# Kernel optimization log

Measured on AMD Instinct MI355X. Metric: run time of the kernel, lower is better.

## Reference

```python
import jax, jax.numpy as jnp
import numpy as np

K_MASK = -2.3819763e+38
NUM_KV_HEADS = 4
SOFT_CAP = 50.0
WINDOW = 1024
ROPE_BASE = 10000.0
ROPE_SCALE = 1.0


def rms_norm(x, scale=None, eps=1e-6):
    var = jnp.mean(jnp.square(x), axis=-1, keepdims=True)
    normed = x * jax.lax.rsqrt(var + eps)
    if scale is not None:
        normed = normed * (1.0 + scale)
    return normed


def apply_rope(x, positions):
    # x: [B, T, N, H], positions: [B, T]
    head_dim = x.shape[-1]
    fraction = 2.0 * jnp.arange(head_dim // 2, dtype=jnp.float32) / head_dim
    timescale = ROPE_BASE ** fraction  # [H/2]
    sinusoid = positions[..., None, None].astype(jnp.float32) / timescale / ROPE_SCALE  # [B,T,1,H/2]
    sin, cos = jnp.sin(sinusoid), jnp.cos(sinusoid)
    first, second = jnp.split(x, 2, axis=-1)
    return jnp.concatenate([first * cos - second * sin,
                            second * cos + first * sin], axis=-1).astype(x.dtype)


def setup_inputs() -> dict:
    key = jax.random.key(0)
    ks = jax.random.split(key, 8)
    B, T, D, N, K, H, F = 2, 2048, 2048, 8, NUM_KV_HEADS, 256, 8192
    CACHE = 4096
    x = jax.random.normal(ks[0], (B, T, D), dtype=jnp.float32)
    segment_pos = jnp.broadcast_to(jnp.arange(T, dtype=jnp.int32)[None, :], (B, T))
    # causal mask over cache slots: after scatter, slot s (< T) holds position s; slots >= T are empty
    s_idx = jnp.arange(CACHE)
    t_idx = jnp.arange(T)
    attn_mask = (s_idx[None, :] <= t_idx[:, None]) & (s_idx[None, :] < T)
    attn_mask = jnp.broadcast_to(attn_mask[None], (B, T, CACHE))
    cache_k = jnp.zeros((B, CACHE, K, H), dtype=jnp.float32)
    cache_v = jnp.zeros((B, CACHE, K, H), dtype=jnp.float32)
    cache_positions = jnp.zeros((B, CACHE), dtype=jnp.int32)
    end_index = jnp.zeros((B,), dtype=jnp.int32)
    w_q = jax.random.normal(ks[1], (N, D, H), dtype=jnp.float32) * 0.02
    w_kv = jax.random.normal(ks[2], (2, K, D, H), dtype=jnp.float32) * 0.02
    w_attn_vec = jax.random.normal(ks[3], (N, H, D), dtype=jnp.float32) * 0.02
    w_gating = jax.random.normal(ks[4], (2, F, D), dtype=jnp.float32) * 0.02
    w_linear = jax.random.normal(ks[5], (F, D), dtype=jnp.float32) * 0.02
    return {
        'x': x, 'segment_pos': segment_pos, 'attn_mask': attn_mask,
        'cache_k': cache_k, 'cache_v': cache_v,
        'cache_positions': cache_positions, 'end_index': end_index,
        'w_q': w_q, 'w_kv': w_kv, 'w_attn_vec': w_attn_vec,
        'q_norm_scale': jnp.zeros((H,), dtype=jnp.float32),
        'k_norm_scale': jnp.zeros((H,), dtype=jnp.float32),
        'pre_attn_scale': jnp.zeros((D,), dtype=jnp.float32),
        'post_attn_scale': jnp.zeros((D,), dtype=jnp.float32),
        'pre_ffw_scale': jnp.zeros((D,), dtype=jnp.float32),
        'post_ffw_scale': jnp.zeros((D,), dtype=jnp.float32),
        'w_gating': w_gating, 'w_linear': w_linear,
        'skip_scale': jnp.ones((1,), dtype=jnp.float32),
    }


def reference(x, segment_pos, attn_mask, cache_k, cache_v, cache_positions, end_index,
              w_q, w_kv, w_attn_vec, q_norm_scale, k_norm_scale,
              pre_attn_scale, post_attn_scale, pre_ffw_scale, post_ffw_scale,
              w_gating, w_linear, skip_scale):
    B, T, D = x.shape
    cache_size = cache_v.shape[1]

    h = rms_norm(x, pre_attn_scale)

    # --- attention ---
    q = jnp.einsum('BTD,NDH->BTNH', h, w_q)
    q = rms_norm(q, q_norm_scale)
    q = apply_rope(q, segment_pos)

    k, v = jnp.einsum('BSD,CKDH->CBSKH', h, w_kv)
    k = rms_norm(k, k_norm_scale)
    v = rms_norm(v, None)
    k = apply_rope(k, segment_pos)

    # KV-cache scatter (ring-buffer indexing)
    idx = (end_index[:, None] + jnp.arange(T)[None, :]) % cache_size  # [B,T]
    bidx = jnp.arange(B)[:, None]
    v = cache_v.at[bidx, idx].set(v)              # [B,S,K,H]
    k = cache_k.at[bidx, idx].set(k)
    cache_pos = cache_positions.at[bidx, idx].set(segment_pos)  # [B,S]

    # GQA logits
    N, H = q.shape[2], q.shape[3]
    G = N // NUM_KV_HEADS
    qg = q.reshape(B, T, NUM_KV_HEADS, G, H)
    logits = jnp.einsum('BTKGH,BSKH->BTKGS', qg, k).reshape(B, T, N, cache_size)

    # soft cap
    logits = jnp.tanh(logits / SOFT_CAP) * SOFT_CAP

    # sliding-window mask against cache positions
    sliding = (cache_pos[:, None, :] > segment_pos[:, :, None] - WINDOW) & \
              (cache_pos[:, None, :] < segment_pos[:, :, None] + WINDOW)  # [B,T,S]
    mask = attn_mask & sliding

    padded = jnp.where(mask[:, :, None, :], logits, K_MASK)
    probs = jax.nn.softmax(padded, axis=-1).astype(k.dtype)

    pg = probs.reshape(B, T, NUM_KV_HEADS, G, cache_size)
    encoded = jnp.einsum('BTKGS,BSKH->BTKGH', pg, v).reshape(B, T, N, H)
    attn_out = jnp.einsum('BTNH,NHD->BTD', encoded, w_attn_vec)

    # post-attn norm + residual (skip_scale on the skip connection)
    attn_out = rms_norm(attn_out, post_attn_scale)
    attn_out = x * skip_scale + attn_out

    # --- feed-forward ---
    ffw_in = rms_norm(attn_out, pre_ffw_scale)
    gate = jnp.einsum('BTF,CHF->BTCH', ffw_in, w_gating)  # C=2
    act = jax.nn.gelu(gate[..., 0, :]) * gate[..., 1, :]
    ffw_out = jnp.einsum('BTH,HF->BTF', act, w_linear)
    ffw_out = rms_norm(ffw_out, post_ffw_scale)

    return attn_out + ffw_out
```

## Files before the change

### kernel.cpp

```cpp
#include <hip/hip_runtime.h>


typedef _Float16 h8 __attribute__((ext_vector_type(8)));
typedef _Float16 h4 __attribute__((ext_vector_type(4)));
typedef float f4 __attribute__((ext_vector_type(4)));

#define BDIM 2
#define TDIM 2048
#define DDIM 2048
#define NQ 8
#define NKV 4
#define HDIM 256
#define FDIM 8192
#define MROWS (BDIM * TDIM)
#define WINDOW 1024
#define QS 4096

__device__ __forceinline__ float gelu_fast(float x) {
  float u = 1.5957691216057308f * (x + 0.044715f * x * x * x);
  float e = __expf(u);
  return x * e / (e + 1.f);
}

__device__ __forceinline__ void g2l16(const _Float16* g, _Float16* l) {
  __builtin_amdgcn_global_load_lds(
      (const __attribute__((address_space(1))) void*)g,
      (__attribute__((address_space(3))) void*)l, 16, 0, 0);
}

__device__ inline float block_sum(float v, float* sbuf) {
#pragma unroll
  for (int off = 32; off; off >>= 1) v += __shfl_xor(v, off, 64);
  __syncthreads();
  if ((threadIdx.x & 63) == 0) sbuf[threadIdx.x >> 6] = v;
  __syncthreads();
  return sbuf[0] + sbuf[1] + sbuf[2] + sbuf[3];
}

template <int EPI>
__global__ __launch_bounds__(256, 3) void gemm_bt(
    const _Float16* __restrict__ A, const _Float16* __restrict__ Bt,
    void* __restrict__ Cout, int M, int Nc, int K) {
  __shared__ _Float16 As[2 * 128 * 32];
  __shared__ _Float16 Bs[2 * 128 * 32];
  const int tid = threadIdx.x;
  const int m0 = blockIdx.y * 128, n0 = blockIdx.x * 128;
  const int w = tid >> 6, lane = tid & 63;
  const int l16 = lane & 15, quad = lane >> 4;
  const int wm = (w >> 1) * 64, wn = (w & 1) * 64;

  f4 acc[4][4];
#pragma unroll
  for (int i = 0; i < 4; i++)
#pragma unroll
    for (int j = 0; j < 4; j++) {
      acc[i][j][0] = 0.f; acc[i][j][1] = 0.f; acc[i][j][2] = 0.f; acc[i][j][3] = 0.f;
    }

  const int lrow = lane >> 2, lcol = (lane & 3) * 8;
  const _Float16* Ag = A + (size_t)(m0 + w * 32 + lrow) * K + lcol;
  const _Float16* Bg = Bt + (size_t)(n0 + w * 32 + lrow) * K + lcol;
  _Float16* AsW = &As[w * 32 * 32];
  _Float16* BsW = &Bs[w * 32 * 32];

  for (int k0 = 0; k0 < K; k0 += 64) {
    __syncthreads();
#pragma unroll
    for (int s = 0; s < 2; s++) {
      g2l16(Ag + k0 + s * 32,                  AsW + s * 4096);
      g2l16(Ag + (size_t)16 * K + k0 + s * 32, AsW + s * 4096 + 16 * 32);
      g2l16(Bg + k0 + s * 32,                  BsW + s * 4096);
      g2l16(Bg + (size_t)16 * K + k0 + s * 32, BsW + s * 4096 + 16 * 32);
    }
    __syncthreads();
#pragma unroll
    for (int s = 0; s < 2; s++) {
      h8 af[4], bf[4];
#pragma unroll
      for (int i = 0; i < 4; i++)
        af[i] = *(const h8*)&As[s * 4096 + (wm + i * 16 + l16) * 32 + quad * 8];
#pragma unroll
      for (int i = 0; i < 4; i++)
        bf[i] = *(const h8*)&Bs[s * 4096 + (wn + i * 16 + l16) * 32 + quad * 8];
#pragma unroll
      for (int mi = 0; mi < 4; mi++)
#pragma unroll
        for (int ni = 0; ni < 4; ni++)
          acc[mi][ni] = __builtin_amdgcn_mfma_f32_16x16x32_f16(af[mi], bf[ni], acc[mi][ni], 0, 0, 0);
    }
  }

#pragma unroll
  for (int mi = 0; mi < 4; mi++)
#pragma unroll
    for (int ni = 0; ni < 4; ni++)
#pragma unroll
      for (int r = 0; r < 4; r++) {
        const int rg = m0 + wm + mi * 16 + quad * 4 + r;
        const int cg = n0 + wn + ni * 16 + l16;
        const size_t idx = (size_t)rg * Nc + cg;
        if (EPI == 0) ((float*)Cout)[idx] = acc[mi][ni][r];
        else          ((_Float16*)Cout)[idx] = (_Float16)acc[mi][ni][r];
      }
}

__global__ __launch_bounds__(256, 2) void gemm_gate(
    const _Float16* __restrict__ A, const _Float16* __restrict__ B0,
    const _Float16* __restrict__ B1, _Float16* __restrict__ act,
    int M, int Nc, int K) {
  __shared__ _Float16 As[2 * 128 * 32];
  __shared__ _Float16 Bs0[2 * 128 * 32];
  __shared__ _Float16 Bs1[2 * 128 * 32];
  const int tid = threadIdx.x;
  const int m0 = blockIdx.y * 128, n0 = blockIdx.x * 128;
  const int w = tid >> 6, lane = tid & 63;
  const int l16 = lane & 15, quad = lane >> 4;
  const int wm = (w >> 1) * 64, wn = (w & 1) * 64;

  f4 acc0[4][4], acc1[4][4];
#pragma unroll
  for (int i = 0; i < 4; i++)
#pragma unroll
    for (int j = 0; j < 4; j++) {
      acc0[i][j][0] = 0.f; acc0[i][j][1] = 0.f; acc0[i][j][2] = 0.f; acc0[i][j][3] = 0.f;
      acc1[i][j][0] = 0.f; acc1[i][j][1] = 0.f; acc1[i][j][2] = 0.f; acc1[i][j][3] = 0.f;
    }

  const int lrow = lane >> 2, lcol = (lane & 3) * 8;
  const _Float16* Ag  = A  + (size_t)(m0 + w * 32 + lrow) * K + lcol;
  const _Float16* B0g = B0 + (size_t)(n0 + w * 32 + lrow) * K + lcol;
  const _Float16* B1g = B1 + (size_t)(n0 + w * 32 + lrow) * K + lcol;
  _Float16* AsW  = &As[w * 32 * 32];
  _Float16* Bs0W = &Bs0[w * 32 * 32];
  _Float16* Bs1W = &Bs1[w * 32 * 32];

  for (int k0 = 0; k0 < K; k0 += 64) {
    __syncthreads();
#pragma unroll
    for (int s = 0; s < 2; s++) {
      g2l16(Ag + k0 + s * 32,                   AsW + s * 4096);
      g2l16(Ag + (size_t)16 * K + k0 + s * 32,  AsW + s * 4096 + 16 * 32);
      g2l16(B0g + k0 + s * 32,                  Bs0W + s * 4096);
      g2l16(B0g + (size_t)16 * K + k0 + s * 32, Bs0W + s * 4096 + 16 * 32);
      g2l16(B1g + k0 + s * 32,                  Bs1W + s * 4096);
      g2l16(B1g + (size_t)16 * K + k0 + s * 32, Bs1W + s * 4096 + 16 * 32);
    }
    __syncthreads();
#pragma unroll
    for (int s = 0; s < 2; s++) {
      h8 af[4], b0f[4], b1f[4];
#pragma unroll
      for (int i = 0; i < 4; i++)
        af[i] = *(const h8*)&As[s * 4096 + (wm + i * 16 + l16) * 32 + quad * 8];
#pragma unroll
      for (int i = 0; i < 4; i++) {
        b0f[i] = *(const h8*)&Bs0[s * 4096 + (wn + i * 16 + l16) * 32 + quad * 8];
        b1f[i] = *(const h8*)&Bs1[s * 4096 + (wn + i * 16 + l16) * 32 + quad * 8];
      }
#pragma unroll
      for (int mi = 0; mi < 4; mi++)
#pragma unroll
        for (int ni = 0; ni < 4; ni++) {
          acc0[mi][ni] = __builtin_amdgcn_mfma_f32_16x16x32_f16(af[mi], b0f[ni], acc0[mi][ni], 0, 0, 0);
          acc1[mi][ni] = __builtin_amdgcn_mfma_f32_16x16x32_f16(af[mi], b1f[ni], acc1[mi][ni], 0, 0, 0);
        }
    }
  }

#pragma unroll
  for (int mi = 0; mi < 4; mi++)
#pragma unroll
    for (int ni = 0; ni < 4; ni++)
#pragma unroll
      for (int r = 0; r < 4; r++) {
        const int rg = m0 + wm + mi * 16 + quad * 4 + r;
        const int cg = n0 + wn + ni * 16 + l16;
        act[(size_t)rg * Nc + cg] =
            (_Float16)(gelu_fast(acc0[mi][ni][r]) * acc1[mi][ni][r]);
      }
}

__global__ __launch_bounds__(256) void transpose_cast_kernel(
    const float* __restrict__ in, _Float16* __restrict__ out,
    int R, int C, size_t in_zstride, size_t out_zstride) {
  __shared__ float tile[64][65];
  const float* ip = in + blockIdx.z * in_zstride;
  _Float16* op = out + blockIdx.z * out_zstride;
  const int cb = blockIdx.x * 64, rb = blockIdx.y * 64;
  const int tx = threadIdx.x & 15, ty = threadIdx.x >> 4;
#pragma unroll
  for (int i = 0; i < 4; i++) {
    f4 v = *(const f4*)&ip[(size_t)(rb + ty + 16 * i) * C + cb + tx * 4];
    tile[ty + 16 * i][tx * 4 + 0] = v[0];
    tile[ty + 16 * i][tx * 4 + 1] = v[1];
    tile[ty + 16 * i][tx * 4 + 2] = v[2];
    tile[ty + 16 * i][tx * 4 + 3] = v[3];
  }
  __syncthreads();
#pragma unroll
  for (int i = 0; i < 4; i++) {
    const int c = ty + 16 * i;
    h4 o;
#pragma unroll
    for (int j = 0; j < 4; j++) o[j] = (_Float16)tile[tx * 4 + j][c];
    *(h4*)&op[(size_t)(cb + c) * R + rb + tx * 4] = o;
  }
}

__global__ void cast_fp16_kernel(const float* __restrict__ in,
                                 _Float16* __restrict__ out, int n4) {
  int i = blockIdx.x * 256 + threadIdx.x;
  if (i < n4) {
    f4 v = ((const f4*)in)[i];
    h4 o;
    o[0] = (_Float16)v[0]; o[1] = (_Float16)v[1];
    o[2] = (_Float16)v[2]; o[3] = (_Float16)v[3];
    ((h4*)out)[i] = o;
  }
}

__global__ __launch_bounds__(256) void rmsnorm_fp16_kernel(
    const float* __restrict__ in, const float* __restrict__ scale,
    _Float16* __restrict__ out) {
  __shared__ float sbuf[4];
  const int row = blockIdx.x, tid = threadIdx.x;
  const float* r = in + (size_t)row * 2048;
  f4 a = ((const f4*)r)[tid];
  f4 b = ((const f4*)r)[tid + 256];
  float ss = a[0]*a[0] + a[1]*a[1] + a[2]*a[2] + a[3]*a[3] +
             b[0]*b[0] + b[1]*b[1] + b[2]*b[2] + b[3]*b[3];
  float tot = block_sum(ss, sbuf);
  float rs = rsqrtf(tot * (1.f / 2048.f) + 1e-6f);
  f4 s0 = ((const f4*)scale)[tid];
  f4 s1 = ((const f4*)scale)[tid + 256];
  h4 o0, o1;
#pragma unroll
  for (int j = 0; j < 4; j++) {
    o0[j] = (_Float16)(a[j] * rs * (1.f + s0[j]));
    o1[j] = (_Float16)(b[j] * rs * (1.f + s1[j]));
  }
  ((h4*)(out + (size_t)row * 2048))[tid] = o0;
  ((h4*)(out + (size_t)row * 2048))[tid + 256] = o1;
}

__global__ __launch_bounds__(256) void headnorm_qkv_kernel(
    const _Float16* __restrict__ qkv, _Float16* __restrict__ out,
    const float* __restrict__ qsc, const float* __restrict__ ksc,
    const int* __restrict__ pos_arr) {
  const int inst = blockIdx.x * 4 + (threadIdx.x >> 6);
  const int lane = threadIdx.x & 63;
  const int row = inst >> 4, slot = inst & 15;
  const _Float16* r = qkv + (size_t)row * QS + slot * 256;
  h4 vh = ((const h4*)r)[lane];
  f4 v;
#pragma unroll
  for (int j = 0; j < 4; j++) v[j] = (float)vh[j];
  float ss = v[0]*v[0] + v[1]*v[1] + v[2]*v[2] + v[3]*v[3];
#pragma unroll
  for (int off = 32; off; off >>= 1) ss += __shfl_xor(ss, off, 64);
  const float rs = rsqrtf(ss * (1.f / 256.f) + 1e-6f);
  const float* scale = (slot < 8) ? qsc : (slot < 12 ? ksc : nullptr);
  f4 nv;
  if (scale) {
    f4 sc = ((const f4*)scale)[lane];
#pragma unroll
    for (int j = 0; j < 4; j++) nv[j] = v[j] * rs * (1.f + sc[j]);
  } else {
#pragma unroll
    for (int j = 0; j < 4; j++) nv[j] = v[j] * rs;
  }
  h4 res;
  if (slot < 12) {
    const float pos = (float)pos_arr[row];
    const bool lo = lane < 32;
#pragma unroll
    for (int j = 0; j < 4; j++) {
      float partner = __shfl_xor(nv[j], 32, 64);
      const int ph = (lane * 4 + j) & 127;
      float it = exp2f((float)ph * -0.103810253f);
      float ang = pos * it;
      float sn, cs;
      sincosf(ang, &sn, &cs);
      res[j] = (_Float16)(lo ? (nv[j] * cs - partner * sn)
                             : (nv[j] * cs + partner * sn));
    }
  } else {
#pragma unroll
    for (int j = 0; j < 4; j++) res[j] = (_Float16)nv[j];
  }
  ((h4*)(out + (size_t)row * QS + slot * 256))[lane] = res;
}

__global__ __launch_bounds__(256) void transpose_v_kernel(
    const _Float16* __restrict__ qkvh, _Float16* __restrict__ vT) {
  __shared__ _Float16 tile[32][33];
  const int z = blockIdx.z;
  const int b = z >> 2, kvh = z & 3;
  const int tb = blockIdx.x * 32, hb = blockIdx.y * 32;
  const int x = threadIdx.x, y = threadIdx.y;
#pragma unroll
  for (int i = 0; i < 4; i++)
    tile[y + 8 * i][x] =
        qkvh[(size_t)(b * TDIM + tb + y + 8 * i) * QS + 3072 + kvh * 256 + hb + x];
  __syncthreads();
#pragma unroll
  for (int i = 0; i < 4; i++)
    vT[((size_t)z * HDIM + hb + y + 8 * i) * TDIM + tb + x] = tile[x][y + 8 * i];
}

__global__ __launch_bounds__(256) void attn_kernel(
    const _Float16* __restrict__ qkvh, const _Float16* __restrict__ vT,
    _Float16* __restrict__ enc) {
  __shared__ _Float16 Ks[32 * 256];
  __shared__ _Float16 Vs[256 * 32];
  __shared__ _Float16 Ps[4][16 * 32];
  const int t0 = blockIdx.x * 64;
  const int n = blockIdx.y;
  const int b = blockIdx.z;
  const int kvh = n >> 1;
  const int tid = threadIdx.x;
  const int w = tid >> 6, lane = tid & 63, l16 = lane & 15, quad = lane >> 4;

  h8 qfrag[8];
  {
    const int trow = t0 + w * 16 + l16;
    const _Float16* qp =
        qkvh + (size_t)(b * TDIM + trow) * QS + n * HDIM + quad * 8;
#pragma unroll
    for (int ks = 0; ks < 8; ks++) qfrag[ks] = *(const h8*)(qp + ks * 32);
  }

  f4 O[16];
#pragma unroll
  for (int i = 0; i < 16; i++) { O[i][0] = 0.f; O[i][1] = 0.f; O[i][2] = 0.f; O[i][3] = 0.f; }
  float m_i[4], l_i[4];
#pragma unroll
  for (int r = 0; r < 4; r++) { m_i[r] = -1e30f; l_i[r] = 0.f; }

  int s_begin = t0 - (WINDOW - 1);
  if (s_begin < 0) s_begin = 0;
  s_begin &= ~31;
  const int s_end = t0 + 64;
  const _Float16* kbase = qkvh + (size_t)b * TDIM * QS + 2048 + kvh * HDIM;
  const _Float16* vbase = vT + ((size_t)(b * NKV + kvh) * HDIM) * TDIM;

  for (int s0 = s_begin; s0 < s_end; s0 += 32) {
    __syncthreads();
#pragma unroll
    for (int p = 0; p < 4; p++) {
      int g = p * 256 + tid;
      {
        int si = g >> 5, hg = (g & 31) << 3;
        *(h8*)&Ks[si * 256 + hg] = *(const h8*)(kbase + (size_t)(s0 + si) * QS + hg);
      }
      {
        int h = g >> 2, sg = (g & 3) << 3;
        *(h8*)&Vs[h * 32 + sg] = *(const h8*)(vbase + (size_t)h * TDIM + s0 + sg);
      }
    }
    __syncthreads();

    float P[2][4], cmax[4];
#pragma unroll
    for (int r = 0; r < 4; r++) cmax[r] = -1e30f;
#pragma unroll
    for (int sc = 0; sc < 2; sc++) {
      f4 lg; lg[0] = 0.f; lg[1] = 0.f; lg[2] = 0.f; lg[3] = 0.f;
#pragma unroll
      for (int ks = 0; ks < 8; ks++) {
        h8 kb = *(const h8*)&Ks[(sc * 16 + l16) * 256 + ks * 32 + quad * 8];
        lg = __builtin_amdgcn_mfma_f32_16x16x32_f16(qfrag[ks], kb, lg, 0, 0, 0);
      }
      const int scol = s0 + sc * 16 + l16;
#pragma unroll
      for (int r = 0; r < 4; r++) {
        const int trow = t0 + w * 16 + quad * 4 + r;
        float t = __expf(lg[r] * 0.04f);
        float xv = 50.f - 100.f * __builtin_amdgcn_rcpf(t + 1.f);
        bool valid = (scol <= trow) && (scol > trow - WINDOW);
        P[sc][r] = valid ? xv : -1e30f;
        cmax[r] = fmaxf(cmax[r], P[sc][r]);
      }
    }
#pragma unroll
    for (int off = 1; off < 16; off <<= 1)
#pragma unroll
      for (int r = 0; r < 4; r++) cmax[r] = fmaxf(cmax[r], __shfl_xor(cmax[r], off, 16));
    float alpha[4], psum[4];
#pragma unroll
    for (int r = 0; r < 4; r++) {
      float mnew = fmaxf(m_i[r], cmax[r]);
      alpha[r] = __expf(m_i[r] - mnew);
      m_i[r] = mnew;
      psum[r] = 0.f;
    }
#pragma unroll
    for (int sc = 0; sc < 2; sc++)
#pragma unroll
      for (int r = 0; r < 4; r++) {
        float pv = __expf(P[sc][r] - m_i[r]);
        P[sc][r] = pv;
        psum[r] += pv;
      }
#pragma unroll
    for (int off = 1; off < 16; off <<= 1)
#pragma unroll
      for (int r = 0; r < 4; r++) psum[r] += __shfl_xor(psum[r], off, 16);
#pragma unroll
    for (int r = 0; r < 4; r++) l_i[r] = l_i[r] * alpha[r] + psum[r];
#pragma unroll
    for (int i = 0; i < 16; i++)
#pragma unroll
      for (int r = 0; r < 4; r++) O[i][r] *= alpha[r];
#pragma unroll
    for (int sc = 0; sc < 2; sc++)
#pragma unroll
      for (int r = 0; r < 4; r++)
        Ps[w][(quad * 4 + r) * 32 + sc * 16 + l16] = (_Float16)P[sc][r];
    h8 pa = *(const h8*)&Ps[w][l16 * 32 + quad * 8];
#pragma unroll
    for (int ht = 0; ht < 16; ht++) {
      h8 vb = *(const h8*)&Vs[(ht * 16 + l16) * 32 + quad * 8];
      O[ht] = __builtin_amdgcn_mfma_f32_16x16x32_f16(pa, vb, O[ht], 0, 0, 0);
    }
  }

  float invl[4];
#pragma unroll
  for (int r = 0; r < 4; r++) invl[r] = 1.f / l_i[r];
#pragma unroll
  for (int ht = 0; ht < 16; ht++)
#pragma unroll
    for (int r = 0; r < 4; r++) {
      const int trow = t0 + w * 16 + quad * 4 + r;
      enc[((size_t)(b * TDIM + trow)) * (NQ * HDIM) + n * HDIM + ht * 16 + l16] =
          (_Float16)(O[ht][r] * invl[r]);
    }
}

__global__ __launch_bounds__(256) void postattn_kernel(
    const float* __restrict__ attnraw, const float* __restrict__ x,
    const float* __restrict__ post_scale, const float* __restrict__ pre_ffw_scale,
    const float* __restrict__ skip, float* __restrict__ attn_out,
    _Float16* __restrict__ ffw_in) {
  __shared__ float sbuf[4];
  const int row = blockIdx.x, tid = threadIdx.x;
  const float* ar = attnraw + (size_t)row * 2048;
  const float* xr = x + (size_t)row * 2048;
  f4 a0 = ((const f4*)ar)[tid], a1 = ((const f4*)ar)[tid + 256];
  float ss = a0[0]*a0[0] + a0[1]*a0[1] + a0[2]*a0[2] + a0[3]*a0[3] +
             a1[0]*a1[0] + a1[1]*a1[1] + a1[2]*a1[2] + a1[3]*a1[3];
  float tot = block_sum(ss, sbuf);
  float rs = rsqrtf(tot * (1.f / 2048.f) + 1e-6f);
  const float sk = skip[0];
  f4 x0 = ((const f4*)xr)[tid], x1 = ((const f4*)xr)[tid + 256];
  f4 p0 = ((const f4*)post_scale)[tid], p1 = ((const f4*)post_scale)[tid + 256];
  f4 at0, at1;
#pragma unroll
  for (int j = 0; j < 4; j++) {
    at0[j] = x0[j] * sk + a0[j] * rs * (1.f + p0[j]);
    at1[j] = x1[j] * sk + a1[j] * rs * (1.f + p1[j]);
  }
  ((f4*)(attn_out + (size_t)row * 2048))[tid] = at0;
  ((f4*)(attn_out + (size_t)row * 2048))[tid + 256] = at1;
  float ss2 = at0[0]*at0[0] + at0[1]*at0[1] + at0[2]*at0[2] + at0[3]*at0[3] +
              at1[0]*at1[0] + at1[1]*at1[1] + at1[2]*at1[2] + at1[3]*at1[3];
  float tot2 = block_sum(ss2, sbuf);
  float rs2 = rsqrtf(tot2 * (1.f / 2048.f) + 1e-6f);
  f4 f0 = ((const f4*)pre_ffw_scale)[tid], f1 = ((const f4*)pre_ffw_scale)[tid + 256];
  h4 o0, o1;
#pragma unroll
  for (int j = 0; j < 4; j++) {
    o0[j] = (_Float16)(at0[j] * rs2 * (1.f + f0[j]));
    o1[j] = (_Float16)(at1[j] * rs2 * (1.f + f1[j]));
  }
  ((h4*)(ffw_in + (size_t)row * 2048))[tid] = o0;
  ((h4*)(ffw_in + (size_t)row * 2048))[tid + 256] = o1;
}

__global__ __launch_bounds__(256) void final_kernel(
    const _Float16* __restrict__ ffw, const float* __restrict__ attn_out,
    const float* __restrict__ post_ffw_scale, float* __restrict__ out) {
  __shared__ float sbuf[4];
  const int row = blockIdx.x, tid = threadIdx.x;
  const _Float16* fr = ffw + (size_t)row * 2048;
  const float* ar = attn_out + (size_t)row * 2048;
  h4 fh0 = ((const h4*)fr)[tid], fh1 = ((const h4*)fr)[tid + 256];
  f4 a0, a1;
#pragma unroll
  for (int j = 0; j < 4; j++) { a0[j] = (float)fh0[j]; a1[j] = (float)fh1[j]; }
  float ss = a0[0]*a0[0] + a0[1]*a0[1] + a0[2]*a0[2] + a0[3]*a0[3] +
             a1[0]*a1[0] + a1[1]*a1[1] + a1[2]*a1[2] + a1[3]*a1[3];
  float tot = block_sum(ss, sbuf);
  float rs = rsqrtf(tot * (1.f / 2048.f) + 1e-6f);
  f4 s0 = ((const f4*)post_ffw_scale)[tid], s1 = ((const f4*)post_ffw_scale)[tid + 256];
  f4 x0 = ((const f4*)ar)[tid], x1 = ((const f4*)ar)[tid + 256];
  f4 o0, o1;
#pragma unroll
  for (int j = 0; j < 4; j++) {
    o0[j] = x0[j] + a0[j] * rs * (1.f + s0[j]);
    o1[j] = x1[j] + a1[j] * rs * (1.f + s1[j]);
  }
  ((f4*)(out + (size_t)row * 2048))[tid] = o0;
  ((f4*)(out + (size_t)row * 2048))[tid + 256] = o1;
}

extern "C" void kernel_launch(void* const* d_in, const int* in_sizes, int n_in,
                              void* d_out, int out_size, void* d_ws, size_t ws_size,
                              hipStream_t stream) {
  (void)in_sizes; (void)n_in; (void)out_size; (void)ws_size;
  const float* x              = (const float*)d_in[0];
  const int*   segment_pos    = (const int*)d_in[1];
  const float* w_q            = (const float*)d_in[7];
  const float* w_kv           = (const float*)d_in[8];
  const float* w_attn_vec     = (const float*)d_in[9];
  const float* q_norm_scale   = (const float*)d_in[10];
  const float* k_norm_scale   = (const float*)d_in[11];
  const float* pre_attn_scale = (const float*)d_in[12];
  const float* post_attn_scale= (const float*)d_in[13];
  const float* pre_ffw_scale  = (const float*)d_in[14];
  const float* post_ffw_scale = (const float*)d_in[15];
  const float* w_gating       = (const float*)d_in[16];
  const float* w_linear       = (const float*)d_in[17];
  const float* skip_scale     = (const float*)d_in[18];

  char* ws = (char*)d_ws;
  const size_t MB = 1024 * 1024;
  _Float16* Wqkv  = (_Float16*)(ws + 0);
  _Float16* Wo    = (_Float16*)(ws + 0);
  _Float16* Wg    = (_Float16*)(ws + 0);
  _Float16* Wl    = (_Float16*)(ws + 0);
  _Float16* Hbf   = (_Float16*)(ws + 64 * MB);
  float* attnF    = (float*)(ws + 80 * MB);
  _Float16* qkvraw= (_Float16*)(ws + 112 * MB);
  _Float16* qkvh  = (_Float16*)(ws + 144 * MB);
  _Float16* enc   = (_Float16*)(ws + 176 * MB);
  float* attnraw  = (float*)(ws + 192 * MB);
  _Float16* vT    = (_Float16*)(ws + 224 * MB);
  _Float16* act   = (_Float16*)(ws + 112 * MB);
  _Float16* ffw   = (_Float16*)(ws + 192 * MB);
  float* outp     = (float*)d_out;

  transpose_cast_kernel<<<dim3(HDIM / 64, DDIM / 64, NQ), 256, 0, stream>>>(
      w_q, Wqkv, DDIM, HDIM, (size_t)DDIM * HDIM, (size_t)HDIM * DDIM);
  transpose_cast_kernel<<<dim3(HDIM / 64, DDIM / 64, NKV), 256, 0, stream>>>(
      w_kv, Wqkv + (size_t)2048 * DDIM, DDIM, HDIM,
      (size_t)DDIM * HDIM, (size_t)HDIM * DDIM);
  transpose_cast_kernel<<<dim3(HDIM / 64, DDIM / 64, NKV), 256, 0, stream>>>(
      w_kv + (size_t)NKV * DDIM * HDIM, Wqkv + (size_t)3072 * DDIM, DDIM, HDIM,
      (size_t)DDIM * HDIM, (size_t)HDIM * DDIM);
  rmsnorm_fp16_kernel<<<MROWS, 256, 0, stream>>>(x, pre_attn_scale, Hbf);
  gemm_bt<1><<<dim3(QS / 128, MROWS / 128), 256, 0, stream>>>(
      Hbf, Wqkv, qkvraw, MROWS, QS, DDIM);
  headnorm_qkv_kernel<<<(MROWS * 16) / 4, 256, 0, stream>>>(
      qkvraw, qkvh, q_norm_scale, k_norm_scale, segment_pos);
  transpose_v_kernel<<<dim3(TDIM / 32, HDIM / 32, BDIM * NKV), dim3(32, 8), 0, stream>>>(
      qkvh, vT);
  attn_kernel<<<dim3(TDIM / 64, NQ, BDIM), 256, 0, stream>>>(qkvh, vT, enc);
  transpose_cast_kernel<<<dim3(DDIM / 64, (NQ * HDIM) / 64, 1), 256, 0, stream>>>(
      w_attn_vec, Wo, NQ * HDIM, DDIM, 0, 0);
  gemm_bt<0><<<dim3(DDIM / 128, MROWS / 128), 256, 0, stream>>>(
      enc, Wo, attnraw, MROWS, DDIM, NQ * HDIM);
  postattn_kernel<<<MROWS, 256, 0, stream>>>(attnraw, x, post_attn_scale,
                                             pre_ffw_scale, skip_scale, attnF, Hbf);
  cast_fp16_kernel<<<(2 * FDIM * DDIM / 4 + 255) / 256, 256, 0, stream>>>(
      w_gating, Wg, 2 * FDIM * DDIM / 4);
  gemm_gate<<<dim3(FDIM / 128, MROWS / 128), 256, 0, stream>>>(
      Hbf, Wg, Wg + (size_t)FDIM * DDIM, act, MROWS, FDIM, DDIM);
  transpose_cast_kernel<<<dim3(DDIM / 64, FDIM / 64, 1), 256, 0, stream>>>(
      w_linear, Wl, FDIM, DDIM, 0, 0);
  gemm_bt<1><<<dim3(DDIM / 128, MROWS / 128), 256, 0, stream>>>(
      act, Wl, ffw, MROWS, DDIM, FDIM);
  final_kernel<<<MROWS, 256, 0, stream>>>(ffw, attnF, post_ffw_scale, outp);
}
```

Baseline: 1.143 ms.

## Rewrite GEMMs as 256x128 triple-buffered swizzled 8-wave kernels; swizzle attention LDS

Replaces the 128x128 double-sync GEMM kernels with 512-thread 256-row tiles that keep a three-stage LDS ring. Global-to-LDS prefetch runs two k-steps ahead, split into phases interleaved with MFMA blocks, and raw s_barrier, s_setprio and explicit vmcnt waits hide load latency. LDS layouts are XOR-swizzled to avoid bank conflicts, and block IDs are remapped to group neighbouring tiles for L2 reuse. The attention kernel's K and V shared-memory tiles get the same XOR swizzle. The hand-tuned waitcnt and barrier ordering adds correctness risk, and the larger LDS footprint may reduce occupancy.

```diff
diff --git a/kernel.cpp b/kernel.cpp
--- a/kernel.cpp
+++ b/kernel.cpp
@@ -16,6 +16,8 @@
 #define WINDOW 1024
 #define QS 4096
 
+#define BAR() asm volatile("s_barrier" ::: "memory")
+
 __device__ __forceinline__ float gelu_fast(float x) {
   float u = 1.5957691216057308f * (x + 0.044715f * x * x * x);
   float e = __expf(u);
@@ -38,16 +40,35 @@
 }
 
 template <int EPI>
-__global__ __launch_bounds__(256, 3) void gemm_bt(
+__global__ __launch_bounds__(512, 2) void gemm256(
     const _Float16* __restrict__ A, const _Float16* __restrict__ Bt,
     void* __restrict__ Cout, int M, int Nc, int K) {
-  __shared__ _Float16 As[2 * 128 * 32];
-  __shared__ _Float16 Bs[2 * 128 * 32];
+  __shared__ _Float16 As[3][256 * 64];
+  __shared__ _Float16 Bs[3][128 * 64];
+  (void)M;
   const int tid = threadIdx.x;
-  const int m0 = blockIdx.y * 128, n0 = blockIdx.x * 128;
-  const int w = tid >> 6, lane = tid & 63;
+  const int lane = tid & 63, w = tid >> 6;
+  const int nwg = gridDim.x;
+  const int bid2 = (blockIdx.x & 7) * (nwg >> 3) + (blockIdx.x >> 3);
+  const int nbx = Nc >> 7;
+  const int bx = bid2 % nbx, by = bid2 / nbx;
+  const int m0 = by * 256, n0 = bx * 128;
+  const int wm = (w >> 1) * 64, wn = (w & 1) * 64;
   const int l16 = lane & 15, quad = lane >> 4;
-  const int wm = (w >> 1) * 64, wn = (w & 1) * 64;
+
+  const int lr = lane >> 3;
+  const int swz8 = ((lane & 7) ^ lr) << 3;
+  const _Float16* Ag = A + (size_t)(m0 + w * 32 + lr) * K + swz8;
+  const _Float16* Bg = Bt + (size_t)(n0 + w * 16 + lr) * K + swz8;
+
+  const int qs8 = (quad ^ (l16 & 3)) << 3;
+  const int kxo = ((l16 >> 2) & 1) << 5;
+  int aoff[4], boff[4];
+#pragma unroll
+  for (int i = 0; i < 4; i++) {
+    aoff[i] = (wm + i * 16 + l16) * 64 + qs8;
+    boff[i] = (wn + i * 16 + l16) * 64 + qs8;
+  }
 
   f4 acc[4][4];
 #pragma unroll
@@ -57,38 +78,69 @@
       acc[i][j][0] = 0.f; acc[i][j][1] = 0.f; acc[i][j][2] = 0.f; acc[i][j][3] = 0.f;
     }
 
-  const int lrow = lane >> 2, lcol = (lane & 3) * 8;
-  const _Float16* Ag = A + (size_t)(m0 + w * 32 + lrow) * K + lcol;
-  const _Float16* Bg = Bt + (size_t)(n0 + w * 32 + lrow) * K + lcol;
-  _Float16* AsW = &As[w * 32 * 32];
-  _Float16* BsW = &Bs[w * 32 * 32];
-
-  for (int k0 = 0; k0 < K; k0 += 64) {
-    __syncthreads();
-#pragma unroll
-    for (int s = 0; s < 2; s++) {
-      g2l16(Ag + k0 + s * 32,                  AsW + s * 4096);
-      g2l16(Ag + (size_t)16 * K + k0 + s * 32, AsW + s * 4096 + 16 * 32);
-      g2l16(Bg + k0 + s * 32,                  BsW + s * 4096);
-      g2l16(Bg + (size_t)16 * K + k0 + s * 32, BsW + s * 4096 + 16 * 32);
-    }
-    __syncthreads();
-#pragma unroll
-    for (int s = 0; s < 2; s++) {
-      h8 af[4], bf[4];
-#pragma unroll
-      for (int i = 0; i < 4; i++)
-        af[i] = *(const h8*)&As[s * 4096 + (wm + i * 16 + l16) * 32 + quad * 8];
-#pragma unroll
-      for (int i = 0; i < 4; i++)
-        bf[i] = *(const h8*)&Bs[s * 4096 + (wn + i * 16 + l16) * 32 + quad * 8];
-#pragma unroll
-      for (int mi = 0; mi < 4; mi++)
-#pragma unroll
-        for (int ni = 0; ni < 4; ni++)
-          acc[mi][ni] = __builtin_amdgcn_mfma_f32_16x16x32_f16(af[mi], bf[ni], acc[mi][ni], 0, 0, 0);
-    }
-  }
+#define SA(b, kt, c) g2l16(Ag + (size_t)(c) * 8 * K + (size_t)(kt) * 64, \
+                           &As[b][(w * 32 + (c) * 8) * 64])
+#define SB(b, kt, c) g2l16(Bg + (size_t)(c) * 8 * K + (size_t)(kt) * 64, \
+                           &Bs[b][(w * 16 + (c) * 8) * 64])
+
+  SA(0, 0, 0); SA(0, 0, 1); SA(0, 0, 2); SA(0, 0, 3); SB(0, 0, 0); SB(0, 0, 1);
+  SA(1, 1, 0); SA(1, 1, 1); SA(1, 1, 2); SA(1, 1, 3); SB(1, 1, 0); SB(1, 1, 1);
+  asm volatile("s_waitcnt vmcnt(6)" ::: "memory");
+  BAR();
+
+  const int nt = K >> 6;
+  for (int kt = 0; kt < nt; ++kt) {
+    const int cur = kt % 3, nb = (kt + 2) % 3;
+    const bool pf = (kt + 2) < nt;
+    const _Float16* Ab = As[cur];
+    const _Float16* Bb = Bs[cur];
+    h8 af[4][2], bf[4][2];
+#pragma unroll
+    for (int i = 0; i < 4; i++) {
+      af[i][0] = *(const h8*)&Ab[aoff[i] + kxo];
+      af[i][1] = *(const h8*)&Ab[aoff[i] + (kxo ^ 32)];
+    }
+#pragma unroll
+    for (int i = 0; i < 2; i++) {
+      bf[i][0] = *(const h8*)&Bb[boff[i] + kxo];
+      bf[i][1] = *(const h8*)&Bb[boff[i] + (kxo ^ 32)];
+    }
+    if (pf) { SA(nb, kt + 2, 0); SA(nb, kt + 2, 1); SA(nb, kt + 2, 2); }
+    BAR();
+    __builtin_amdgcn_s_setprio(1);
+#pragma unroll
+    for (int mi = 0; mi < 4; mi++)
+#pragma unroll
+      for (int ni = 0; ni < 2; ni++)
+#pragma unroll
+        for (int ks = 0; ks < 2; ks++)
+          acc[mi][ni] = __builtin_amdgcn_mfma_f32_16x16x32_f16(
+              af[mi][ks], bf[ni][ks], acc[mi][ni], 0, 0, 0);
+    __builtin_amdgcn_s_setprio(0);
+    BAR();
+#pragma unroll
+    for (int i = 2; i < 4; i++) {
+      bf[i][0] = *(const h8*)&Bb[boff[i] + kxo];
+      bf[i][1] = *(const h8*)&Bb[boff[i] + (kxo ^ 32)];
+    }
+    if (pf) { SA(nb, kt + 2, 3); SB(nb, kt + 2, 0); SB(nb, kt + 2, 1); }
+    BAR();
+    __builtin_amdgcn_s_setprio(1);
+#pragma unroll
+    for (int mi = 0; mi < 4; mi++)
+#pragma unroll
+      for (int ni = 2; ni < 4; ni++)
+#pragma unroll
+        for (int ks = 0; ks < 2; ks++)
+          acc[mi][ni] = __builtin_amdgcn_mfma_f32_16x16x32_f16(
+              af[mi][ks], bf[ni][ks], acc[mi][ni], 0, 0, 0);
+    __builtin_amdgcn_s_setprio(0);
+    if (pf)                 asm volatile("s_waitcnt vmcnt(6)" ::: "memory");
+    else if (kt + 2 == nt)  asm volatile("s_waitcnt vmcnt(0)" ::: "memory");
+    BAR();
+  }
+#undef SA
+#undef SB
 
 #pragma unroll
   for (int mi = 0; mi < 4; mi++)
@@ -104,73 +156,117 @@
       }
 }
 
-__global__ __launch_bounds__(256, 2) void gemm_gate(
+__global__ __launch_bounds__(512, 2) void gemm_gate256(
     const _Float16* __restrict__ A, const _Float16* __restrict__ B0,
     const _Float16* __restrict__ B1, _Float16* __restrict__ act,
     int M, int Nc, int K) {
-  __shared__ _Float16 As[2 * 128 * 32];
-  __shared__ _Float16 Bs0[2 * 128 * 32];
-  __shared__ _Float16 Bs1[2 * 128 * 32];
+  __shared__ _Float16 As[3][256 * 64];
+  __shared__ _Float16 B0s[3][64 * 64];
+  __shared__ _Float16 B1s[3][64 * 64];
+  (void)M;
   const int tid = threadIdx.x;
-  const int m0 = blockIdx.y * 128, n0 = blockIdx.x * 128;
-  const int w = tid >> 6, lane = tid & 63;
+  const int lane = tid & 63, w = tid >> 6;
+  const int nwg = gridDim.x;
+  const int bid2 = (blockIdx.x & 7) * (nwg >> 3) + (blockIdx.x >> 3);
+  const int nbx = Nc >> 6;
+  const int bx = bid2 % nbx, by = bid2 / nbx;
+  const int m0 = by * 256, n0 = bx * 64;
+  const int wm = (w >> 1) * 64, wn = (w & 1) * 32;
   const int l16 = lane & 15, quad = lane >> 4;
-  const int wm = (w >> 1) * 64, wn = (w & 1) * 64;
-
-  f4 acc0[4][4], acc1[4][4];
+
+  const int lr = lane >> 3;
+  const int swz8 = ((lane & 7) ^ lr) << 3;
+  const _Float16* Ag  = A  + (size_t)(m0 + w * 32 + lr) * K + swz8;
+  const _Float16* B0g = B0 + (size_t)(n0 + w * 8 + lr) * K + swz8;
+  const _Float16* B1g = B1 + (size_t)(n0 + w * 8 + lr) * K + swz8;
+
+  const int qs8 = (quad ^ (l16 & 3)) << 3;
+  const int kxo = ((l16 >> 2) & 1) << 5;
+  int aoff[4], boff[2];
+#pragma unroll
+  for (int i = 0; i < 4; i++) aoff[i] = (wm + i * 16 + l16) * 64 + qs8;
+#pragma unroll
+  for (int i = 0; i < 2; i++) boff[i] = (wn + i * 16 + l16) * 64 + qs8;
+
+  f4 acc0[4][2], acc1[4][2];
 #pragma unroll
   for (int i = 0; i < 4; i++)
 #pragma unroll
-    for (int j = 0; j < 4; j++) {
+    for (int j = 0; j < 2; j++) {
       acc0[i][j][0] = 0.f; acc0[i][j][1] = 0.f; acc0[i][j][2] = 0.f; acc0[i][j][3] = 0.f;
       acc1[i][j][0] = 0.f; acc1[i][j][1] = 0.f; acc1[i][j][2] = 0.f; acc1[i][j][3] = 0.f;
     }
 
-  const int lrow = lane >> 2, lcol = (lane & 3) * 8;
-  const _Float16* Ag  = A  + (size_t)(m0 + w * 32 + lrow) * K + lcol;
-  const _Float16* B0g = B0 + (size_t)(n0 + w * 32 + lrow) * K + lcol;
-  const _Float16* B1g = B1 + (size_t)(n0 + w * 32 + lrow) * K + lcol;
-  _Float16* AsW  = &As[w * 32 * 32];
-  _Float16* Bs0W = &Bs0[w * 32 * 32];
-  _Float16* Bs1W = &Bs1[w * 32 * 32];
-
-  for (int k0 = 0; k0 < K; k0 += 64) {
-    __syncthreads();
-#pragma unroll
-    for (int s = 0; s < 2; s++) {
-      g2l16(Ag + k0 + s * 32,                   AsW + s * 4096);
-      g2l16(Ag + (size_t)16 * K + k0 + s * 32,  AsW + s * 4096 + 16 * 32);
-      g2l16(B0g + k0 + s * 32,                  Bs0W + s * 4096);
-      g2l16(B0g + (size_t)16 * K + k0 + s * 32, Bs0W + s * 4096 + 16 * 32);
-      g2l16(B1g + k0 + s * 32,                  Bs1W + s * 4096);
-      g2l16(B1g + (size_t)16 * K + k0 + s * 32, Bs1W + s * 4096 + 16 * 32);
-    }
-    __syncthreads();
-#pragma unroll
-    for (int s = 0; s < 2; s++) {
-      h8 af[4], b0f[4], b1f[4];
-#pragma unroll
-      for (int i = 0; i < 4; i++)
-        af[i] = *(const h8*)&As[s * 4096 + (wm + i * 16 + l16) * 32 + quad * 8];
-#pragma unroll
-      for (int i = 0; i < 4; i++) {
-        b0f[i] = *(const h8*)&Bs0[s * 4096 + (wn + i * 16 + l16) * 32 + quad * 8];
-        b1f[i] = *(const h8*)&Bs1[s * 4096 + (wn + i * 16 + l16) * 32 + quad * 8];
-      }
-#pragma unroll
-      for (int mi = 0; mi < 4; mi++)
-#pragma unroll
-        for (int ni = 0; ni < 4; ni++) {
-          acc0[mi][ni] = __builtin_amdgcn_mfma_f32_16x16x32_f16(af[mi], b0f[ni], acc0[mi][ni], 0, 0, 0);
-          acc1[mi][ni] = __builtin_amdgcn_mfma_f32_16x16x32_f16(af[mi], b1f[ni], acc1[mi][ni], 0, 0, 0);
-        }
-    }
-  }
+#define SA(b, kt, c) g2l16(Ag + (size_t)(c) * 8 * K + (size_t)(kt) * 64, \
+                           &As[b][(w * 32 + (c) * 8) * 64])
+#define SB0(b, kt) g2l16(B0g + (size_t)(kt) * 64, &B0s[b][w * 8 * 64])
+#define SB1(b, kt) g2l16(B1g + (size_t)(kt) * 64, &B1s[b][w * 8 * 64])
+
+  SA(0, 0, 0); SA(0, 0, 1); SA(0, 0, 2); SA(0, 0, 3); SB0(0, 0); SB1(0, 0);
+  SA(1, 1, 0); SA(1, 1, 1); SA(1, 1, 2); SA(1, 1, 3); SB0(1, 1); SB1(1, 1);
+  asm volatile("s_waitcnt vmcnt(6)" ::: "memory");
+  BAR();
+
+  const int nt = K >> 6;
+  for (int kt = 0; kt < nt; ++kt) {
+    const int cur = kt % 3, nb = (kt + 2) % 3;
+    const bool pf = (kt + 2) < nt;
+    const _Float16* Ab = As[cur];
+    const _Float16* Bb0 = B0s[cur];
+    const _Float16* Bb1 = B1s[cur];
+    h8 af[4][2], b0f[2][2], b1f[2][2];
+#pragma unroll
+    for (int i = 0; i < 4; i++) {
+      af[i][0] = *(const h8*)&Ab[aoff[i] + kxo];
+      af[i][1] = *(const h8*)&Ab[aoff[i] + (kxo ^ 32)];
+    }
+#pragma unroll
+    for (int i = 0; i < 2; i++) {
+      b0f[i][0] = *(const h8*)&Bb0[boff[i] + kxo];
+      b0f[i][1] = *(const h8*)&Bb0[boff[i] + (kxo ^ 32)];
+    }
+    if (pf) { SA(nb, kt + 2, 0); SA(nb, kt + 2, 1); SA(nb, kt + 2, 2); }
+    BAR();
+    __builtin_amdgcn_s_setprio(1);
+#pragma unroll
+    for (int mi = 0; mi < 4; mi++)
+#pragma unroll
+      for (int ni = 0; ni < 2; ni++)
+#pragma unroll
+        for (int ks = 0; ks < 2; ks++)
+          acc0[mi][ni] = __builtin_amdgcn_mfma_f32_16x16x32_f16(
+              af[mi][ks], b0f[ni][ks], acc0[mi][ni], 0, 0, 0);
+    __builtin_amdgcn_s_setprio(0);
+    BAR();
+#pragma unroll
+    for (int i = 0; i < 2; i++) {
+      b1f[i][0] = *(const h8*)&Bb1[boff[i] + kxo];
+      b1f[i][1] = *(const h8*)&Bb1[boff[i] + (kxo ^ 32)];
+    }
+    if (pf) { SA(nb, kt + 2, 3); SB0(nb, kt + 2); SB1(nb, kt + 2); }
+    BAR();
+    __builtin_amdgcn_s_setprio(1);
+#pragma unroll
+    for (int mi = 0; mi < 4; mi++)
+#pragma unroll
+      for (int ni = 0; ni < 2; ni++)
+#pragma unroll
+        for (int ks = 0; ks < 2; ks++)
+          acc1[mi][ni] = __builtin_amdgcn_mfma_f32_16x16x32_f16(
+              af[mi][ks], b1f[ni][ks], acc1[mi][ni], 0, 0, 0);
+    __builtin_amdgcn_s_setprio(0);
+    if (pf)                 asm volatile("s_waitcnt vmcnt(6)" ::: "memory");
+    else if (kt + 2 == nt)  asm volatile("s_waitcnt vmcnt(0)" ::: "memory");
+    BAR();
+  }
+#undef SA
+#undef SB0
+#undef SB1
 
 #pragma unroll
   for (int mi = 0; mi < 4; mi++)
 #pragma unroll
-    for (int ni = 0; ni < 4; ni++)
+    for (int ni = 0; ni < 2; ni++)
 #pragma unroll
       for (int r = 0; r < 4; r++) {
         const int rg = m0 + wm + mi * 16 + quad * 4 + r;
@@ -320,6 +416,9 @@
   const int kvh = n >> 1;
   const int tid = threadIdx.x;
   const int w = tid >> 6, lane = tid & 63, l16 = lane & 15, quad = lane >> 4;
+  const int kxr = (l16 >> 2) & 1;
+  const int qsK8 = (quad ^ (l16 & 3)) << 3;
+  const int qsV8 = (quad ^ ((l16 >> 1) & 3)) << 3;
 
   h8 qfrag[8];
   {
@@ -350,12 +449,14 @@
     for (int p = 0; p < 4; p++) {
       int g = p * 256 + tid;
       {
-        int si = g >> 5, hg = (g & 31) << 3;
-        *(h8*)&Ks[si * 256 + hg] = *(const h8*)(kbase + (size_t)(s0 + si) * QS + hg);
+        int si = g >> 5, c = g & 31;
+        *(h8*)&Ks[si * 256 + ((c ^ (si & 7)) << 3)] =
+            *(const h8*)(kbase + (size_t)(s0 + si) * QS + (c << 3));
       }
       {
-        int h = g >> 2, sg = (g & 3) << 3;
-        *(h8*)&Vs[h * 32 + sg] = *(const h8*)(vbase + (size_t)h * TDIM + s0 + sg);
+        int h = g >> 2, c = g & 3;
+        *(h8*)&Vs[h * 32 + ((c ^ ((g >> 3) & 3)) << 3)] =
+            *(const h8*)(vbase + (size_t)h * TDIM + s0 + (c << 3));
       }
     }
     __syncthreads();
@@ -368,7 +469,7 @@
       f4 lg; lg[0] = 0.f; lg[1] = 0.f; lg[2] = 0.f; lg[3] = 0.f;
 #pragma unroll
       for (int ks = 0; ks < 8; ks++) {
-        h8 kb = *(const h8*)&Ks[(sc * 16 + l16) * 256 + ks * 32 + quad * 8];
+        h8 kb = *(const h8*)&Ks[(sc * 16 + l16) * 256 + ((ks ^ kxr) << 5) + qsK8];
         lg = __builtin_amdgcn_mfma_f32_16x16x32_f16(qfrag[ks], kb, lg, 0, 0, 0);
       }
       const int scol = s0 + sc * 16 + l16;
@@ -420,7 +521,7 @@
     h8 pa = *(const h8*)&Ps[w][l16 * 32 + quad * 8];
 #pragma unroll
     for (int ht = 0; ht < 16; ht++) {
-      h8 vb = *(const h8*)&Vs[(ht * 16 + l16) * 32 + quad * 8];
+      h8 vb = *(const h8*)&Vs[(ht * 16 + l16) * 32 + qsV8];
       O[ht] = __builtin_amdgcn_mfma_f32_16x16x32_f16(pa, vb, O[ht], 0, 0, 0);
     }
   }
@@ -550,7 +651,7 @@
       w_kv + (size_t)NKV * DDIM * HDIM, Wqkv + (size_t)3072 * DDIM, DDIM, HDIM,
       (size_t)DDIM * HDIM, (size_t)HDIM * DDIM);
   rmsnorm_fp16_kernel<<<MROWS, 256, 0, stream>>>(x, pre_attn_scale, Hbf);
-  gemm_bt<1><<<dim3(QS / 128, MROWS / 128), 256, 0, stream>>>(
+  gemm256<1><<<dim3((QS / 128) * (MROWS / 256)), 512, 0, stream>>>(
       Hbf, Wqkv, qkvraw, MROWS, QS, DDIM);
   headnorm_qkv_kernel<<<(MROWS * 16) / 4, 256, 0, stream>>>(
       qkvraw, qkvh, q_norm_scale, k_norm_scale, segment_pos);
@@ -559,17 +660,17 @@
   attn_kernel<<<dim3(TDIM / 64, NQ, BDIM), 256, 0, stream>>>(qkvh, vT, enc);
   transpose_cast_kernel<<<dim3(DDIM / 64, (NQ * HDIM) / 64, 1), 256, 0, stream>>>(
       w_attn_vec, Wo, NQ * HDIM, DDIM, 0, 0);
-  gemm_bt<0><<<dim3(DDIM / 128, MROWS / 128), 256, 0, stream>>>(
+  gemm256<0><<<dim3((DDIM / 128) * (MROWS / 256)), 512, 0, stream>>>(
       enc, Wo, attnraw, MROWS, DDIM, NQ * HDIM);
   postattn_kernel<<<MROWS, 256, 0, stream>>>(attnraw, x, post_attn_scale,
                                              pre_ffw_scale, skip_scale, attnF, Hbf);
   cast_fp16_kernel<<<(2 * FDIM * DDIM / 4 + 255) / 256, 256, 0, stream>>>(
       w_gating, Wg, 2 * FDIM * DDIM / 4);
-  gemm_gate<<<dim3(FDIM / 128, MROWS / 128), 256, 0, stream>>>(
+  gemm_gate256<<<dim3((FDIM / 64) * (MROWS / 256)), 512, 0, stream>>>(
       Hbf, Wg, Wg + (size_t)FDIM * DDIM, act, MROWS, FDIM, DDIM);
   transpose_cast_kernel<<<dim3(DDIM / 64, FDIM / 64, 1), 256, 0, stream>>>(
       w_linear, Wl, FDIM, DDIM, 0, 0);
-  gemm_bt<1><<<dim3(DDIM / 128, MROWS / 128), 256, 0, stream>>>(
+  gemm256<1><<<dim3((DDIM / 128) * (MROWS / 256)), 512, 0, stream>>>(
       act, Wl, ffw, MROWS, DDIM, FDIM);
   final_kernel<<<MROWS, 256, 0, stream>>>(ffw, attnF, post_ffw_scale, outp);
 }
```

Measured after the change: 1.159 ms. Within noise of the previous version (+1.4%).
